# Kernel optimization log

Measured on AMD Instinct MI355X. Metric: run time of the kernel, lower is better.

Reference implementation:

```python
import jax, jax.numpy as jnp
import numpy as np

B = 8          # number of point clouds
P = 2048       # points per cloud (equal-length segments)
D_FEAT = 16    # matched feature dim
BIG = 1e10     # mask value for cross-batch pairs

LOSS_WEIGHT = 1.0
COORD_WEIGHT = 1.0
FEAT_WEIGHT = 0.1


def setup_inputs() -> dict:
    key = jax.random.key(0)
    k1, k2, k3, k4 = jax.random.split(key, 4)
    n = B * P
    pred_coord = jax.random.normal(k1, (n, 3), dtype=jnp.float32) * 10.0
    target_coord = jax.random.normal(k2, (n, 3), dtype=jnp.float32) * 10.0
    pred_feat = jax.random.normal(k3, (n, D_FEAT), dtype=jnp.float32)
    target_feat = jax.random.normal(k4, (n, D_FEAT), dtype=jnp.float32)
    offsets = (jnp.arange(1, B + 1) * P).astype(jnp.int32)  # cumulative ends
    return {
        'pred_coord': pred_coord,
        'target_coord': target_coord,
        'pred_feat': pred_feat,
        'target_feat': target_feat,
        'pred_offset': offsets,
        'target_offset': offsets,
    }


def _batch_ids(offsets, n):
    # point i belongs to batch b where offsets[b-1] <= i < offsets[b]
    return jnp.searchsorted(offsets, jnp.arange(n), side='right')


def _lengths(offsets):
    prev = jnp.concatenate([jnp.zeros((1,), offsets.dtype), offsets[:-1]])
    return offsets - prev


def _nn_dist(x, y, xb, yb):
    # masked all-pairs squared distances [n, m]; per-batch KNN(k=1)
    d2 = (jnp.sum(x * x, axis=1)[:, None]
          - 2.0 * (x @ y.T)
          + jnp.sum(y * y, axis=1)[None, :])
    d2 = jnp.where(xb[:, None] == yb[None, :], d2, BIG)
    idx = jnp.argmin(d2, axis=1)
    nearest = y[idx]                          # gather nearest neighbor
    dist = jnp.sum((x - nearest) ** 2, axis=1)  # norm=2, recomputed as in torch
    return dist, idx


def _chamfer_dir(x, y, x_off, y_off):
    xb = _batch_ids(x_off, x.shape[0])
    yb = _batch_ids(y_off, y.shape[0])
    dist, idx = _nn_dist(x, y, xb, yb)
    seg = jax.ops.segment_sum(dist, xb, num_segments=B)
    lens = jnp.maximum(_lengths(x_off), 1).astype(dist.dtype)
    return seg / lens, idx                    # point_reduction='mean'


def reference(pred_coord, target_coord, pred_feat, target_feat,
              pred_offset, target_offset):
    cham_x, x_idx = _chamfer_dir(pred_coord, target_coord, pred_offset, target_offset)
    cham_y, _ = _chamfer_dir(target_coord, pred_coord, target_offset, pred_offset)
    # bidirectional sum, batch_reduction='mean' (weights None -> divide by B)
    coord_loss = jnp.sum(cham_x + cham_y) / B
    # matched feature MSE via pred->target nearest-neighbor indices
    nearest_feat = target_feat[x_idx]
    feat_loss = jnp.mean((pred_feat - nearest_feat) ** 2)
    loss = LOSS_WEIGHT * (COORD_WEIGHT * coord_loss + FEAT_WEIGHT * feat_loss)
    return (loss, coord_loss, feat_loss)
```

## Files before the change

### kernel.cpp

```cpp
#include <hip/hip_runtime.h>

#define BATCHES 8
#define PTS     2048
#define DFEAT   16
#define NQ      16384
#define NBLK    512

__global__ __launch_bounds__(512, 4) void
nn_fused_kernel(const float* __restrict__ pred_coord,
                const float* __restrict__ target_coord,
                const float* __restrict__ pred_feat,
                const float* __restrict__ target_feat,
                float2* __restrict__ partials) {
    __shared__ float4 cand[2048];
    __shared__ unsigned long long pk[8][64];
    __shared__ unsigned long long fk[64];
    __shared__ float wa[8], wb[8];

    const int bid   = blockIdx.x;
    const int dir   = bid >> 8;
    const int rem   = bid & 255;
    const int batch = rem >> 5;
    const int qg    = rem & 31;
    const int tid   = threadIdx.x;
    const int lane  = tid & 63;
    const int slice = tid >> 6;

    const float* x = (dir == 0) ? pred_coord   : target_coord;
    const float* y = (dir == 0) ? target_coord : pred_coord;

    const float* ybase = y + (size_t)batch * PTS * 3;
    #pragma unroll
    for (int r = 0; r < 4; ++r) {
        int k = tid + 512 * r;
        float cx = ybase[3 * k], cy = ybase[3 * k + 1], cz = ybase[3 * k + 2];
        cand[k] = make_float4(cx, cy, cz, 0.5f * (cx * cx + cy * cy + cz * cz));
    }

    const int qbase = batch * PTS + qg * 64;
    const int q = qbase + lane;
    float ax = x[3 * q], ay = x[3 * q + 1], az = x[3 * q + 2];
    const float nax = -ax, nay = -ay, naz = -az;
    const float hx  = 0.5f * (ax * ax + ay * ay + az * az);

    __syncthreads();

    const int jbase = slice * 256;
    float best = 1e30f;
    int   bj   = 0;
    if (dir == 0) {
        #pragma unroll 8
        for (int i = 0; i < 256; ++i) {
            float4 c = cand[jbase + i];
            float s = fmaf(nax, c.x,
                      fmaf(nay, c.y,
                      fmaf(naz, c.z, c.w)));
            if (s < best) { best = s; bj = i; }
        }
    } else {
        #pragma unroll 8
        for (int i = 0; i < 256; ++i) {
            float4 c = cand[jbase + i];
            float s = fmaf(nax, c.x,
                      fmaf(nay, c.y,
                      fmaf(naz, c.z, c.w)));
            best = fminf(best, s);
        }
    }
    pk[slice][lane] =
        ((unsigned long long)__float_as_uint(fmaxf(best + hx, 0.f)) << 32)
        | (unsigned int)(jbase + bj);
    __syncthreads();

    float ds = 0.f, fs = 0.f;
    if (tid < 64) {
        unsigned long long m = pk[0][tid];
        #pragma unroll
        for (int c = 1; c < 8; ++c) {
            unsigned long long v = pk[c][tid];
            m = (v < m) ? v : m;
        }
        fk[tid] = m;
        ds = 2.0f * __uint_as_float((unsigned int)(m >> 32));
    }
    __syncthreads();

    if (dir == 0 && tid < 256) {
        const unsigned long long m = fk[tid >> 2];
        const int row = batch * PTS + (int)(m & 0xffffffffu);
        const float4* pf = (const float4*)(pred_feat + (size_t)(qbase + (tid >> 2)) * DFEAT);
        const float4* tf = (const float4*)(target_feat + (size_t)row * DFEAT);
        float4 a = pf[tid & 3], b = tf[tid & 3];
        float d0 = a.x - b.x, d1 = a.y - b.y, d2 = a.z - b.z, d3 = a.w - b.w;
        fs = d0 * d0 + d1 * d1 + d2 * d2 + d3 * d3;
    }

    #pragma unroll
    for (int off = 32; off > 0; off >>= 1) {
        ds += __shfl_down(ds, off);
        fs += __shfl_down(fs, off);
    }
    if (lane == 0) { wa[slice] = ds; wb[slice] = fs; }
    __syncthreads();
    if (tid == 0) {
        float a = 0.f, b = 0.f;
        #pragma unroll
        for (int w = 0; w < 8; ++w) { a += wa[w]; b += wb[w]; }
        partials[bid] = make_float2(a, b);
    }
}

__global__ __launch_bounds__(512) void
final_kernel(const float2* __restrict__ partials, float* __restrict__ out) {
    __shared__ float a8[8], b8[8];
    const int tid = threadIdx.x;
    float2 p = partials[tid];
    float ds = p.x, fs = p.y;
    #pragma unroll
    for (int off = 32; off > 0; off >>= 1) {
        ds += __shfl_down(ds, off);
        fs += __shfl_down(fs, off);
    }
    const int wave = tid >> 6, lane = tid & 63;
    if (lane == 0) { a8[wave] = ds; b8[wave] = fs; }
    __syncthreads();
    if (tid == 0) {
        float dsum = 0.f, fsum = 0.f;
        #pragma unroll
        for (int w = 0; w < 8; ++w) { dsum += a8[w]; fsum += b8[w]; }
        float coord_loss = dsum / (float)(BATCHES * PTS);
        float feat_loss  = fsum / (float)(NQ * DFEAT);
        out[0] = coord_loss + 0.1f * feat_loss;
        out[1] = coord_loss;
        out[2] = feat_loss;
    }
}

extern "C" void kernel_launch(void* const* d_in, const int* in_sizes, int n_in,
                              void* d_out, int out_size, void* d_ws, size_t ws_size,
                              hipStream_t stream) {
    const float* pred_coord   = (const float*)d_in[0];
    const float* target_coord = (const float*)d_in[1];
    const float* pred_feat    = (const float*)d_in[2];
    const float* target_feat  = (const float*)d_in[3];

    float2* partials = (float2*)d_ws;

    nn_fused_kernel<<<NBLK, 512, 0, stream>>>(pred_coord, target_coord,
                                              pred_feat, target_feat, partials);
    final_kernel<<<1, 512, 0, stream>>>(partials, (float*)d_out);
}
```

Before: 88.91 us.

## Register-block four queries per thread to reuse each LDS candidate load

Each thread now evaluates four query points against every candidate it loads from shared memory, instead of one. Within a wave, lanes are split into four groups, each taking a strided quarter of the slice's candidates. The per-query partial minima are then merged across waves and groups through a larger shared array. This cuts LDS reads per FMA by four, at the cost of more registers and a wider final reduction. Ties between equal distances may now pick a different neighbour index than before.

After: 74.33 us (median of 2 runs). -16.4%, faster.

```diff
diff --git a/kernel.cpp b/kernel.cpp
--- a/kernel.cpp
+++ b/kernel.cpp
@@ -13,7 +13,7 @@
                 const float* __restrict__ target_feat,
                 float2* __restrict__ partials) {
     __shared__ float4 cand[2048];
-    __shared__ unsigned long long pk[8][64];
+    __shared__ unsigned long long pk[8][4][4][16];
     __shared__ unsigned long long fk[64];
     __shared__ float wa[8], wb[8];
 
@@ -25,6 +25,8 @@
     const int tid   = threadIdx.x;
     const int lane  = tid & 63;
     const int slice = tid >> 6;
+    const int g     = lane >> 4;
+    const int q16   = lane & 15;
 
     const float* x = (dir == 0) ? pred_coord   : target_coord;
     const float* y = (dir == 0) ? target_coord : pred_coord;
@@ -38,48 +40,64 @@
     }
 
     const int qbase = batch * PTS + qg * 64;
-    const int q = qbase + lane;
-    float ax = x[3 * q], ay = x[3 * q + 1], az = x[3 * q + 2];
-    const float nax = -ax, nay = -ay, naz = -az;
-    const float hx  = 0.5f * (ax * ax + ay * ay + az * az);
+    float nax[4], nay[4], naz[4], hx[4];
+    #pragma unroll
+    for (int k = 0; k < 4; ++k) {
+        int q = qbase + q16 + 16 * k;
+        float ax = x[3 * q], ay = x[3 * q + 1], az = x[3 * q + 2];
+        nax[k] = -ax; nay[k] = -ay; naz[k] = -az;
+        hx[k]  = 0.5f * (ax * ax + ay * ay + az * az);
+    }
 
     __syncthreads();
 
-    const int jbase = slice * 256;
-    float best = 1e30f;
-    int   bj   = 0;
+    const int jbase = slice * 256 + g;
+    float best[4] = {1e30f, 1e30f, 1e30f, 1e30f};
+    int   bj[4]   = {0, 0, 0, 0};
     if (dir == 0) {
         #pragma unroll 8
-        for (int i = 0; i < 256; ++i) {
-            float4 c = cand[jbase + i];
-            float s = fmaf(nax, c.x,
-                      fmaf(nay, c.y,
-                      fmaf(naz, c.z, c.w)));
-            if (s < best) { best = s; bj = i; }
+        for (int i = 0; i < 64; ++i) {
+            int j = jbase + 4 * i;
+            float4 c = cand[j];
+            #pragma unroll
+            for (int k = 0; k < 4; ++k) {
+                float s = fmaf(nax[k], c.x,
+                          fmaf(nay[k], c.y,
+                          fmaf(naz[k], c.z, c.w)));
+                if (s < best[k]) { best[k] = s; bj[k] = j; }
+            }
         }
     } else {
         #pragma unroll 8
-        for (int i = 0; i < 256; ++i) {
-            float4 c = cand[jbase + i];
-            float s = fmaf(nax, c.x,
-                      fmaf(nay, c.y,
-                      fmaf(naz, c.z, c.w)));
-            best = fminf(best, s);
+        for (int i = 0; i < 64; ++i) {
+            float4 c = cand[jbase + 4 * i];
+            #pragma unroll
+            for (int k = 0; k < 4; ++k) {
+                float s = fmaf(nax[k], c.x,
+                          fmaf(nay[k], c.y,
+                          fmaf(naz[k], c.z, c.w)));
+                best[k] = fminf(best[k], s);
+            }
         }
     }
-    pk[slice][lane] =
-        ((unsigned long long)__float_as_uint(fmaxf(best + hx, 0.f)) << 32)
-        | (unsigned int)(jbase + bj);
+    #pragma unroll
+    for (int k = 0; k < 4; ++k) {
+        pk[slice][g][k][q16] =
+            ((unsigned long long)__float_as_uint(fmaxf(best[k] + hx[k], 0.f)) << 32)
+            | (unsigned int)bj[k];
+    }
     __syncthreads();
 
     float ds = 0.f, fs = 0.f;
     if (tid < 64) {
-        unsigned long long m = pk[0][tid];
+        unsigned long long m = ~0ull;
         #pragma unroll
-        for (int c = 1; c < 8; ++c) {
-            unsigned long long v = pk[c][tid];
-            m = (v < m) ? v : m;
-        }
+        for (int w = 0; w < 8; ++w)
+            #pragma unroll
+            for (int gg = 0; gg < 4; ++gg) {
+                unsigned long long v = pk[w][gg][tid >> 4][tid & 15];
+                m = (v < m) ? v : m;
+            }
         fk[tid] = m;
         ds = 2.0f * __uint_as_float((unsigned int)(m >> 32));
     }
```
